# Kernel optimization log

Hardware: AMD Instinct MI355X
Metric: run time of the kernel (lower is better)

Reference implementation:

```python
import jax, jax.numpy as jnp
import numpy as np

N_NODES = 4_000_000
N_GRAPHS = 4096  # B; fixed for jit (torch derives it from batch.max()+1)
D_FEAT = 8
NUM_CLASSES = 10


def setup_inputs() -> dict:
    key = jax.random.key(0)
    k1, k2, k3, k4, k5 = jax.random.split(key, 5)
    x = jax.random.normal(k1, (N_NODES, D_FEAT), dtype=jnp.float32)
    # sorted segment ids; with ~977 nodes/graph expected, empty segments are vanishingly unlikely
    batch_ids = jnp.sort(jax.random.randint(k2, (N_NODES,), 0, N_GRAPHS, dtype=jnp.int64))
    input_ids = jax.random.randint(k3, (N_GRAPHS, 128), 0, 30522, dtype=jnp.int64)
    attention_mask = jnp.ones((N_GRAPHS, 128), dtype=jnp.int64)
    W = jax.random.normal(k4, (NUM_CLASSES, D_FEAT), dtype=jnp.float32) * (1.0 / np.sqrt(D_FEAT))
    b = jax.random.normal(k5, (NUM_CLASSES,), dtype=jnp.float32) * 0.01
    return {"x": x, "batch_ids": batch_ids, "input_ids": input_ids,
            "attention_mask": attention_mask, "W": W, "b": b}


def reference(x, batch_ids, input_ids, attention_mask, W, b):
    # Segment-mean pooling: replaces the O(B) python loop of masked means
    # with a single-pass scatter-add. input_ids / attention_mask are unused
    # by the original forward (kept for signature fidelity).
    sums = jax.ops.segment_sum(x, batch_ids, num_segments=N_GRAPHS)          # [B, 8]
    counts = jax.ops.segment_sum(jnp.ones((x.shape[0],), x.dtype), batch_ids,
                                 num_segments=N_GRAPHS)                      # [B]
    pooled = sums / counts[:, None]                                          # [B, 8]
    logits = pooled @ W.T + b                                                # [B, 10]
    return logits
```

## Files before the change

### kernel.cpp

```cpp
#include <hip/hip_runtime.h>

constexpr int N_NODES  = 4000000;
constexpr int N_GRAPHS = 4096;
constexpr int D_FEAT   = 8;
constexpr int N_CLS    = 10;

__global__ __launch_bounds__(256) void find_bounds(
    const int* __restrict__ ids, int* __restrict__ bounds)
{
    int g = blockIdx.x * blockDim.x + threadIdx.x;
    if (g > N_GRAPHS) return;
    int lo = 0, hi = N_NODES;
    while (lo < hi) {
        int mid = (lo + hi) >> 1;
        if (ids[mid] < g) lo = mid + 1; else hi = mid;
    }
    bounds[g] = lo;
}

__global__ __launch_bounds__(256) void pool_linear(
    const float4* __restrict__ x4,
    const int*    __restrict__ bounds,
    const float*  __restrict__ W,
    const float*  __restrict__ bias,
    float*        __restrict__ out)
{
    int g = blockIdx.x;
    int s = bounds[g];
    int e = bounds[g + 1];
    int len = e - s;

    float4 a0 = make_float4(0.f, 0.f, 0.f, 0.f);
    float4 a1 = make_float4(0.f, 0.f, 0.f, 0.f);

    for (int n = s + (int)threadIdx.x; n < e; n += 256) {
        float4 v0 = x4[2 * (size_t)n];
        float4 v1 = x4[2 * (size_t)n + 1];
        a0.x += v0.x; a0.y += v0.y; a0.z += v0.z; a0.w += v0.w;
        a1.x += v1.x; a1.y += v1.y; a1.z += v1.z; a1.w += v1.w;
    }

    #pragma unroll
    for (int off = 32; off > 0; off >>= 1) {
        a0.x += __shfl_xor(a0.x, off);
        a0.y += __shfl_xor(a0.y, off);
        a0.z += __shfl_xor(a0.z, off);
        a0.w += __shfl_xor(a0.w, off);
        a1.x += __shfl_xor(a1.x, off);
        a1.y += __shfl_xor(a1.y, off);
        a1.z += __shfl_xor(a1.z, off);
        a1.w += __shfl_xor(a1.w, off);
    }

    __shared__ float red[4][D_FEAT];
    __shared__ float mean[D_FEAT];
    int wid  = threadIdx.x >> 6;
    int lane = threadIdx.x & 63;
    if (lane == 0) {
        red[wid][0] = a0.x; red[wid][1] = a0.y;
        red[wid][2] = a0.z; red[wid][3] = a0.w;
        red[wid][4] = a1.x; red[wid][5] = a1.y;
        red[wid][6] = a1.z; red[wid][7] = a1.w;
    }
    __syncthreads();
    if (threadIdx.x < D_FEAT) {
        float v = red[0][threadIdx.x] + red[1][threadIdx.x]
                + red[2][threadIdx.x] + red[3][threadIdx.x];
        mean[threadIdx.x] = v / (float)len;
    }
    __syncthreads();
    if (threadIdx.x < N_CLS) {
        const float* w = W + (size_t)threadIdx.x * D_FEAT;
        float acc = bias[threadIdx.x];
        #pragma unroll
        for (int j = 0; j < D_FEAT; ++j)
            acc += mean[j] * w[j];
        out[(size_t)g * N_CLS + threadIdx.x] = acc;
    }
}

extern "C" void kernel_launch(void* const* d_in, const int* in_sizes, int n_in,
                              void* d_out, int out_size, void* d_ws, size_t ws_size,
                              hipStream_t stream) {
    const float* x   = (const float*)d_in[0];
    const int*   ids = (const int*)d_in[1];
    const float* W   = (const float*)d_in[4];
    const float* b   = (const float*)d_in[5];
    float*       out = (float*)d_out;

    int* bounds = (int*)d_ws;

    find_bounds<<<(N_GRAPHS + 1 + 255) / 256, 256, 0, stream>>>(ids, bounds);
    pool_linear<<<N_GRAPHS, 256, 0, stream>>>((const float4*)x, bounds, W, b, out);
}
```

Baseline: 33.98 us.

## Replace binary-search bounds with linear boundary scan and nontemporal loads

The per-graph binary search over segment ids is replaced by a kernel where each thread reads four ids and writes the start offsets for any segment boundaries it sees. The pooling kernel also switches to ext_vector_type arithmetic and nontemporal loads for the feature stream. The scan reads the full 16MB id array instead of doing a few thousand log-depth searches, trading latency-bound dependent loads for a bandwidth-bound pass, which may cost more. The scan also relies on every segment being non-empty or on the write loops covering the gaps.

```diff
diff --git a/kernel.cpp b/kernel.cpp
--- a/kernel.cpp
+++ b/kernel.cpp
@@ -5,39 +5,51 @@
 constexpr int D_FEAT   = 8;
 constexpr int N_CLS    = 10;
 
-__global__ __launch_bounds__(256) void find_bounds(
-    const int* __restrict__ ids, int* __restrict__ bounds)
+typedef float f32x4 __attribute__((ext_vector_type(4)));
+typedef int   i32x4 __attribute__((ext_vector_type(4)));
+
+__global__ __launch_bounds__(256) void scan_bounds(
+    const i32x4* __restrict__ ids4, const int* __restrict__ ids,
+    int* __restrict__ bounds)
 {
-    int g = blockIdx.x * blockDim.x + threadIdx.x;
-    if (g > N_GRAPHS) return;
-    int lo = 0, hi = N_NODES;
-    while (lo < hi) {
-        int mid = (lo + hi) >> 1;
-        if (ids[mid] < g) lo = mid + 1; else hi = mid;
+    int t = blockIdx.x * blockDim.x + threadIdx.x;
+    int base = t * 4;
+    if (base >= N_NODES) return;
+
+    i32x4 v = __builtin_nontemporal_load(ids4 + t);
+    int prev = (base == 0) ? -1 : ids[base - 1];
+
+    int cur;
+    cur = v.x; if (cur != prev) { for (int g = prev + 1; g <= cur; ++g) bounds[g] = base + 0; } prev = cur;
+    cur = v.y; if (cur != prev) { for (int g = prev + 1; g <= cur; ++g) bounds[g] = base + 1; } prev = cur;
+    cur = v.z; if (cur != prev) { for (int g = prev + 1; g <= cur; ++g) bounds[g] = base + 2; } prev = cur;
+    cur = v.w; if (cur != prev) { for (int g = prev + 1; g <= cur; ++g) bounds[g] = base + 3; } prev = cur;
+
+    if (base + 4 >= N_NODES) {
+        for (int g = prev + 1; g <= N_GRAPHS; ++g) bounds[g] = N_NODES;
     }
-    bounds[g] = lo;
 }
 
 __global__ __launch_bounds__(256) void pool_linear(
-    const float4* __restrict__ x4,
-    const int*    __restrict__ bounds,
-    const float*  __restrict__ W,
-    const float*  __restrict__ bias,
-    float*        __restrict__ out)
+    const f32x4* __restrict__ x4,
+    const int*   __restrict__ bounds,
+    const float* __restrict__ W,
+    const float* __restrict__ bias,
+    float*       __restrict__ out)
 {
     int g = blockIdx.x;
     int s = bounds[g];
     int e = bounds[g + 1];
     int len = e - s;
 
-    float4 a0 = make_float4(0.f, 0.f, 0.f, 0.f);
-    float4 a1 = make_float4(0.f, 0.f, 0.f, 0.f);
+    f32x4 a0 = (f32x4)(0.f);
+    f32x4 a1 = (f32x4)(0.f);
 
     for (int n = s + (int)threadIdx.x; n < e; n += 256) {
-        float4 v0 = x4[2 * (size_t)n];
-        float4 v1 = x4[2 * (size_t)n + 1];
-        a0.x += v0.x; a0.y += v0.y; a0.z += v0.z; a0.w += v0.w;
-        a1.x += v1.x; a1.y += v1.y; a1.z += v1.z; a1.w += v1.w;
+        f32x4 v0 = __builtin_nontemporal_load(x4 + 2 * (size_t)n);
+        f32x4 v1 = __builtin_nontemporal_load(x4 + 2 * (size_t)n + 1);
+        a0 += v0;
+        a1 += v1;
     }
 
     #pragma unroll
@@ -90,6 +102,8 @@
 
     int* bounds = (int*)d_ws;
 
-    find_bounds<<<(N_GRAPHS + 1 + 255) / 256, 256, 0, stream>>>(ids, bounds);
-    pool_linear<<<N_GRAPHS, 256, 0, stream>>>((const float4*)x, bounds, W, b, out);
+    int scan_threads = N_NODES / 4;
+    scan_bounds<<<(scan_threads + 255) / 256, 256, 0, stream>>>(
+        (const i32x4*)ids, ids, bounds);
+    pool_linear<<<N_GRAPHS, 256, 0, stream>>>((const f32x4*)x, bounds, W, b, out);
 }
```

Result: no change. 34.10 us (+0.4%).
